# Kernel tuning notes

Measured on AMD Instinct MI355X. Metric: run time of the kernel, lower is better.

## Reference

```python
import jax, jax.numpy as jnp
import numpy as np

N = 50000        # nodes
E = 1_600_000    # edges
F_IN = 128
HID = 128
OUT = 128
NEG_SLOPE = 0.2  # PyG GATConv default


def _gat_layer(x, src, dst, W, a_src, a_dst, b, n_nodes):
    """PyG GATConv (heads=1, add_self_loops handled by caller)."""
    h = x @ W                                   # [N, d_out]
    alpha_src = h @ a_src                       # [N]
    alpha_dst = h @ a_dst                       # [N]
    e = jax.nn.leaky_relu(alpha_src[src] + alpha_dst[dst], NEG_SLOPE)  # [E']
    # segment softmax over incoming edges of each destination node
    m = jax.ops.segment_max(e, dst, num_segments=n_nodes)
    e = jnp.exp(e - m[dst])
    s = jax.ops.segment_sum(e, dst, num_segments=n_nodes)
    alpha = e / s[dst]                          # [E']
    out = jax.ops.segment_sum(alpha[:, None] * h[src], dst, num_segments=n_nodes)
    return out + b


def setup_inputs() -> dict:
    key = jax.random.key(0)
    ks = jax.random.split(key, 11)
    sW1 = 1.0 / np.sqrt(F_IN)
    sW2 = 1.0 / np.sqrt(HID)
    return {
        "x": jax.random.normal(ks[0], (N, F_IN), dtype=jnp.float32),
        "edge_index": jax.random.randint(ks[1], (2, E), 0, N, dtype=jnp.int64
                                         if jax.config.jax_enable_x64 else jnp.int32),
        "W1": jax.random.normal(ks[2], (F_IN, HID), dtype=jnp.float32) * sW1,
        "a1_src": jax.random.normal(ks[3], (HID,), dtype=jnp.float32) * sW2,
        "a1_dst": jax.random.normal(ks[4], (HID,), dtype=jnp.float32) * sW2,
        "b1": jnp.zeros((HID,), dtype=jnp.float32),
        "W2": jax.random.normal(ks[5], (HID, OUT), dtype=jnp.float32) * sW2,
        "a2_src": jax.random.normal(ks[6], (OUT,), dtype=jnp.float32) * sW2,
        "a2_dst": jax.random.normal(ks[7], (OUT,), dtype=jnp.float32) * sW2,
        "b2": jnp.zeros((OUT,), dtype=jnp.float32),
    }


def reference(x, edge_index, W1, a1_src, a1_dst, b1, W2, a2_src, a2_dst, b2):
    n = x.shape[0]
    loop = jnp.arange(n, dtype=edge_index.dtype)
    src = jnp.concatenate([edge_index[0], loop])   # add self loops (PyG default)
    dst = jnp.concatenate([edge_index[1], loop])
    h = _gat_layer(x, src, dst, W1, a1_src, a1_dst, b1, n)
    h = jax.nn.relu(h)
    # F.dropout with training=False is identity (eval-mode reference)
    out = _gat_layer(h, src, dst, W2, a2_src, a2_dst, b2, n)
    return out
```

## Files before the change

### kernel.cpp

```cpp
#include <hip/hip_runtime.h>
#include <hip/hip_bf16.h>
#include <hip/hip_fp16.h>

#define FD 128
#define CBW 64
#define NB_MAX 1024

typedef _Float16 half8 __attribute__((ext_vector_type(8)));
typedef float f32x4 __attribute__((ext_vector_type(4)));

__global__ __launch_bounds__(256) void k_chist(const int* __restrict__ dst,
                                               int* __restrict__ ccnt, int e, int nb) {
    __shared__ int lh[NB_MAX];
    for (int i = threadIdx.x; i < nb; i += 256) lh[i] = 0;
    __syncthreads();
    for (int i = blockIdx.x * 256 + threadIdx.x; i < e; i += gridDim.x * 256)
        atomicAdd(&lh[dst[i] >> 6], 1);
    __syncthreads();
    for (int i = threadIdx.x; i < nb; i += 256) {
        int c = lh[i];
        if (c) atomicAdd(&ccnt[i], c);
    }
}

__global__ void k_cscan(const int* __restrict__ ccnt, int* __restrict__ cbase,
                        int* __restrict__ ccur, int nb, int* __restrict__ rowptr, int n) {
    __shared__ int wsum[16];
    __shared__ int woff[17];
    const int t = threadIdx.x, lane = t & 63, wid = t >> 6;
    int carry = 0;
    for (int base = 0; base < nb; base += 1024) {
        int idx = base + t;
        int v = (idx < nb) ? ccnt[idx] : 0;
        int s = v;
#pragma unroll
        for (int off = 1; off < 64; off <<= 1) {
            int u = __shfl_up(s, off, 64);
            if (lane >= off) s += u;
        }
        if (lane == 63) wsum[wid] = s;
        __syncthreads();
        if (wid == 0) {
            int w2 = (lane < 16) ? wsum[lane] : 0;
#pragma unroll
            for (int off = 1; off < 16; off <<= 1) {
                int u = __shfl_up(w2, off, 64);
                if (lane >= off) w2 += u;
            }
            if (lane < 16) woff[lane + 1] = w2;
            if (lane == 0) woff[0] = 0;
        }
        __syncthreads();
        int excl = carry + woff[wid] + (s - v);
        if (idx < nb) { cbase[idx] = excl; ccur[idx] = excl; }
        carry += woff[16];
        __syncthreads();
    }
    if (t == 0) { cbase[nb] = carry; rowptr[n] = carry; }
}

__global__ __launch_bounds__(256) void k_cscatter(const int* __restrict__ src,
                                                  const int* __restrict__ dst,
                                                  int* __restrict__ ccur,
                                                  int* __restrict__ ebuf,
                                                  int e, int nb, int nblocks) {
    __shared__ int lh[NB_MAX];
    __shared__ int lb[NB_MAX];
    const int per = (e + nblocks - 1) / nblocks;
    const int lo = blockIdx.x * per;
    const int hi = min(e, lo + per);
    const int t = threadIdx.x;
    for (int i = t; i < nb; i += 256) lh[i] = 0;
    __syncthreads();
    for (int i = lo + t; i < hi; i += 256) atomicAdd(&lh[dst[i] >> 6], 1);
    __syncthreads();
    for (int i = t; i < nb; i += 256) {
        int c = lh[i];
        lb[i] = c ? atomicAdd(&ccur[i], c) : 0;
    }
    __syncthreads();
    for (int i = t; i < nb; i += 256) lh[i] = 0;
    __syncthreads();
    for (int i = lo + t; i < hi; i += 256) {
        int d = dst[i];
        int bkt = d >> 6;
        int r = atomicAdd(&lh[bkt], 1);
        ebuf[lb[bkt] + r] = (src[i] << 6) | (d & (CBW - 1));
    }
}

__global__ __launch_bounds__(256) void k_fine(const int* __restrict__ ebuf,
                                              const int* __restrict__ cbase,
                                              int* __restrict__ rowptr,
                                              int* __restrict__ colidx, int n) {
    const int b = blockIdx.x;
    const int node0 = b * CBW;
    const int nloc = min(CBW, n - node0);
    const int beg = cbase[b], end = cbase[b + 1];
    __shared__ int fh[CBW];
    __shared__ int fo[CBW];
    const int t = threadIdx.x;
    if (t < CBW) fh[t] = 0;
    __syncthreads();
    for (int e = beg + t; e < end; e += 256) atomicAdd(&fh[ebuf[e] & (CBW - 1)], 1);
    __syncthreads();
    if (t < 64) {
        int v = fh[t];
        int s = v;
#pragma unroll
        for (int off = 1; off < 64; off <<= 1) {
            int u = __shfl_up(s, off, 64);
            if (t >= off) s += u;
        }
        fo[t] = s - v;
    }
    __syncthreads();
    if (t < nloc) rowptr[node0 + t] = beg + fo[t];
    if (t < CBW) fh[t] = 0;
    __syncthreads();
    for (int e = beg + t; e < end; e += 256) {
        int v = ebuf[e];
        int d = v & (CBW - 1);
        int r = atomicAdd(&fh[d], 1);
        colidx[beg + fo[d] + r] = v >> 6;
    }
}

__global__ __launch_bounds__(1024) void k_wt(const float* __restrict__ Wa,
                                             const float* __restrict__ Wb,
                                             __half* __restrict__ Ta,
                                             __half* __restrict__ Tb) {
    __shared__ float sw[128 * 129];
    const float* W = blockIdx.x ? Wb : Wa;
    __half* T = blockIdx.x ? Tb : Ta;
    const int t = threadIdx.x;
#pragma unroll
    for (int i = 0; i < 16; i++) {
        int idx = i * 1024 + t;
        sw[(idx >> 7) * 129 + (idx & 127)] = W[idx];
    }
    __syncthreads();
#pragma unroll
    for (int i = 0; i < 8; i++) {
        int o = i * 1024 + t;
        int c = o >> 6, kp = o & 63;
        float lo = sw[(kp * 2) * 129 + c];
        float hi = sw[(kp * 2 + 1) * 129 + c];
        *(__half2*)&T[c * 128 + kp * 2] = __floats2half2_rn(lo, hi);
    }
}

__global__ __launch_bounds__(256) void k_gemm(const float* __restrict__ X,
                                              const __half* __restrict__ Wt,
                                              const float* __restrict__ a_s,
                                              const float* __restrict__ a_d,
                                              __half* __restrict__ H,
                                              float* __restrict__ as_,
                                              float* __restrict__ ad_, int n) {
    const int t = threadIdx.x;
    const int wave = t >> 6, lane = t & 63;
    const int g = lane >> 4, c16 = lane & 15;
    const int row0 = blockIdx.x * 64 + wave * 16;

    half8 A[4];
    {
        int row = row0 + c16;
        int rc = (row < n) ? row : (n - 1);
        const float* xp = &X[(size_t)rc * 128 + g * 8];
#pragma unroll
        for (int kc = 0; kc < 4; kc++) {
            float4 x0 = *(const float4*)(xp + kc * 32);
            float4 x1 = *(const float4*)(xp + kc * 32 + 4);
            half8 a;
            a[0] = (_Float16)x0.x; a[1] = (_Float16)x0.y;
            a[2] = (_Float16)x0.z; a[3] = (_Float16)x0.w;
            a[4] = (_Float16)x1.x; a[5] = (_Float16)x1.y;
            a[6] = (_Float16)x1.z; a[7] = (_Float16)x1.w;
            A[kc] = a;
        }
    }

    f32x4 acc[8];
#pragma unroll
    for (int ct = 0; ct < 8; ct++) acc[ct] = (f32x4){0.f, 0.f, 0.f, 0.f};

#pragma unroll
    for (int ct = 0; ct < 8; ct++) {
        const __half* wp = &Wt[(ct * 16 + c16) * 128 + g * 8];
#pragma unroll
        for (int kc = 0; kc < 4; kc++) {
            half8 b = *(const half8*)(wp + kc * 32);
            acc[ct] = __builtin_amdgcn_mfma_f32_16x16x32_f16(A[kc], b, acc[ct], 0, 0, 0);
        }
    }

    float asv[8], adv[8];
#pragma unroll
    for (int ct = 0; ct < 8; ct++) {
        asv[ct] = a_s[ct * 16 + c16];
        adv[ct] = a_d[ct * 16 + c16];
    }
#pragma unroll
    for (int r = 0; r < 4; r++) {
        const int row = row0 + g * 4 + r;
        float vs = 0.f, vd = 0.f;
#pragma unroll
        for (int ct = 0; ct < 8; ct++) {
            float v = acc[ct][r];
            vs += v * asv[ct];
            vd += v * adv[ct];
            if (row < n) H[(size_t)row * 128 + ct * 16 + c16] = __float2half(v);
        }
#pragma unroll
        for (int off = 8; off; off >>= 1) {
            vs += __shfl_xor(vs, off, 16);
            vd += __shfl_xor(vd, off, 16);
        }
        if (c16 == 0 && row < n) { as_[row] = vs; ad_[row] = vd; }
    }
}

__global__ __launch_bounds__(256) void k_aggr(const __half* __restrict__ H,
                                              const float* __restrict__ as_,
                                              const float* __restrict__ ad_,
                                              const int* __restrict__ rowptr,
                                              const int* __restrict__ colidx,
                                              const float* __restrict__ bias,
                                              float* __restrict__ out, int n, int do_relu) {
    const int wid = threadIdx.x >> 6;
    const int lane = threadIdx.x & 63;
    const int node = blockIdx.x * 4 + wid;
    if (node >= n) return;
    const int q = lane >> 4;
    const int l = lane & 15;
    const int f0 = l * 8;
    const float adn = ad_[node];
    float s_acc = 0.f;
    float a0 = 0.f, a1 = 0.f, a2 = 0.f, a3 = 0.f, a4 = 0.f, a5 = 0.f, a6 = 0.f, a7 = 0.f;
    const int beg = rowptr[node], end = rowptr[node + 1];
    int i = beg + q;
    int src_n = 0; float as_n = 0.f;
    if (i < end) { src_n = colidx[i]; as_n = as_[src_n]; }
    while (i < end) {
        const int src_c = src_n; const float as_c = as_n;
        const uint4 hv = *(const uint4*)&H[(size_t)src_c * 128 + f0];
        const int i2 = i + 4;
        if (i2 < end) { src_n = colidx[i2]; as_n = as_[src_n]; }
        float e = as_c + adn;
        e = (e > 0.f) ? e : 0.2f * e;
        const float w = __expf(e);
        s_acc += w;
        float2 p;
        p = __half22float2(*(const __half2*)&hv.x); a0 += w * p.x; a1 += w * p.y;
        p = __half22float2(*(const __half2*)&hv.y); a2 += w * p.x; a3 += w * p.y;
        p = __half22float2(*(const __half2*)&hv.z); a4 += w * p.x; a5 += w * p.y;
        p = __half22float2(*(const __half2*)&hv.w); a6 += w * p.x; a7 += w * p.y;
        i = i2;
    }
    if (q == 3) {
        float e = as_[node] + adn;
        e = (e > 0.f) ? e : 0.2f * e;
        const float w = __expf(e);
        s_acc += w;
        const uint4 hv = *(const uint4*)&H[(size_t)node * 128 + f0];
        float2 p;
        p = __half22float2(*(const __half2*)&hv.x); a0 += w * p.x; a1 += w * p.y;
        p = __half22float2(*(const __half2*)&hv.y); a2 += w * p.x; a3 += w * p.y;
        p = __half22float2(*(const __half2*)&hv.z); a4 += w * p.x; a5 += w * p.y;
        p = __half22float2(*(const __half2*)&hv.w); a6 += w * p.x; a7 += w * p.y;
    }
#pragma unroll
    for (int off = 16; off <= 32; off <<= 1) {
        s_acc += __shfl_xor(s_acc, off);
        a0 += __shfl_xor(a0, off); a1 += __shfl_xor(a1, off);
        a2 += __shfl_xor(a2, off); a3 += __shfl_xor(a3, off);
        a4 += __shfl_xor(a4, off); a5 += __shfl_xor(a5, off);
        a6 += __shfl_xor(a6, off); a7 += __shfl_xor(a7, off);
    }
    if (q == 0) {
        const float inv = 1.f / s_acc;
        const float4 b0 = *(const float4*)&bias[f0];
        const float4 b1 = *(const float4*)&bias[f0 + 4];
        float4 o0, o1;
        o0.x = a0 * inv + b0.x; o0.y = a1 * inv + b0.y;
        o0.z = a2 * inv + b0.z; o0.w = a3 * inv + b0.w;
        o1.x = a4 * inv + b1.x; o1.y = a5 * inv + b1.y;
        o1.z = a6 * inv + b1.z; o1.w = a7 * inv + b1.w;
        if (do_relu) {
            o0.x = fmaxf(o0.x, 0.f); o0.y = fmaxf(o0.y, 0.f);
            o0.z = fmaxf(o0.z, 0.f); o0.w = fmaxf(o0.w, 0.f);
            o1.x = fmaxf(o1.x, 0.f); o1.y = fmaxf(o1.y, 0.f);
            o1.z = fmaxf(o1.z, 0.f); o1.w = fmaxf(o1.w, 0.f);
        }
        *(float4*)&out[(size_t)node * 128 + f0] = o0;
        *(float4*)&out[(size_t)node * 128 + f0 + 4] = o1;
    }
}

extern "C" void kernel_launch(void* const* d_in, const int* in_sizes, int n_in,
                              void* d_out, int out_size, void* d_ws, size_t ws_size,
                              hipStream_t stream) {
    const float* x   = (const float*)d_in[0];
    const int*   ei  = (const int*)d_in[1];
    const float* W1  = (const float*)d_in[2];
    const float* a1s = (const float*)d_in[3];
    const float* a1d = (const float*)d_in[4];
    const float* b1  = (const float*)d_in[5];
    const float* W2  = (const float*)d_in[6];
    const float* a2s = (const float*)d_in[7];
    const float* a2d = (const float*)d_in[8];
    const float* b2  = (const float*)d_in[9];
    float* dout = (float*)d_out;

    const int n = in_sizes[0] / FD;
    const int E = in_sizes[1] / 2;
    const int* src = ei;
    const int* dst = ei + E;
    const int NB = (n + CBW - 1) / CBW;

    __half* H     = (__half*)d_ws;
    int*    ebuf  = (int*)d_ws;
    float* as_    = (float*)((char*)d_ws + (size_t)n * FD * sizeof(__half));
    float* ad_    = as_ + n;
    int*   rowptr = (int*)(ad_ + n);
    int*   ccnt   = rowptr + (n + 1);
    int*   cbase  = ccnt + NB;
    int*   ccur   = cbase + NB + 1;
    int*   colidx = ccur + NB;
    size_t wt_off = (((size_t)((char*)(colidx + E) - (char*)d_ws)) + 15) & ~(size_t)15;
    __half* Wt1h  = (__half*)((char*)d_ws + wt_off);
    __half* Wt2h  = Wt1h + 128 * 128;

    k_wt<<<2, 1024, 0, stream>>>(W1, W2, Wt1h, Wt2h);
    hipMemsetAsync(ccnt, 0, (size_t)NB * sizeof(int), stream);
    k_chist<<<256, 256, 0, stream>>>(dst, ccnt, E, NB);
    k_cscan<<<1, 1024, 0, stream>>>(ccnt, cbase, ccur, NB, rowptr, n);
    const int SCAT_BLOCKS = 256;
    k_cscatter<<<SCAT_BLOCKS, 256, 0, stream>>>(src, dst, ccur, ebuf, E, NB, SCAT_BLOCKS);
    k_fine<<<NB, 256, 0, stream>>>(ebuf, cbase, rowptr, colidx, n);

    const int gemm_grid = (n + 63) / 64;
    const int node_grid = (n + 3) / 4;

    k_gemm<<<gemm_grid, 256, 0, stream>>>(x, Wt1h, a1s, a1d, H, as_, ad_, n);
    k_aggr<<<node_grid, 256, 0, stream>>>(H, as_, ad_, rowptr, colidx, b1, dout, n, 1);

    k_gemm<<<gemm_grid, 256, 0, stream>>>(dout, Wt2h, a2s, a2d, H, as_, ad_, n);
    k_aggr<<<node_grid, 256, 0, stream>>>(H, as_, ad_, rowptr, colidx, b2, dout, n, 0);
}
```

Baseline: 254.7 us.

## Precompute normalized attention weights in separate kernel and unroll aggregation by two

Adds a k_alpha kernel that computes per-edge exp-leaky-relu scores, normalizes them per destination and stores alpha per edge plus the self-loop weight. The aggregation kernel then reads precomputed alpha instead of gathering as_[src] and computing exp inline. It also processes two edges per lane group per iteration so more H row loads are in flight. This removes the dependent as_ gather from the latency-bound aggregation loop, at the cost of an extra kernel launch and extra per-edge alpha writes and reads.

```diff
diff --git a/kernel.cpp b/kernel.cpp
--- a/kernel.cpp
+++ b/kernel.cpp
@@ -220,9 +220,47 @@
     }
 }
 
+__global__ __launch_bounds__(256) void k_alpha(const float* __restrict__ as_,
+                                               const float* __restrict__ ad_,
+                                               const int* __restrict__ rowptr,
+                                               const int* __restrict__ colidx,
+                                               float* __restrict__ alpha,
+                                               float* __restrict__ aself, int n) {
+    const int wid = threadIdx.x >> 6;
+    const int lane = threadIdx.x & 63;
+    const int node = blockIdx.x * 4 + wid;
+    if (node >= n) return;
+    const float adn = ad_[node];
+    const int beg = rowptr[node], end = rowptr[node + 1];
+    float s = 0.f;
+    for (int i = beg + lane; i < end; i += 64) {
+        float e = as_[colidx[i]] + adn;
+        e = (e > 0.f) ? e : 0.2f * e;
+        float w = __expf(e);
+        alpha[i] = w;
+        s += w;
+    }
+    float es = as_[node] + adn;
+    es = (es > 0.f) ? es : 0.2f * es;
+    const float wself = __expf(es);
+    if (lane == 0) s += wself;
+#pragma unroll
+    for (int off = 32; off; off >>= 1) s += __shfl_xor(s, off);
+    const float inv = 1.f / s;
+    for (int i = beg + lane; i < end; i += 64) alpha[i] *= inv;
+    if (lane == 0) aself[node] = wself * inv;
+}
+
+__device__ __forceinline__ void fmix8(float* acc, uint4 hv, float w) {
+    union { uint4 u; _Float16 h[8]; } c;
+    c.u = hv;
+#pragma unroll
+    for (int j = 0; j < 8; j++) acc[j] += w * (float)c.h[j];
+}
+
 __global__ __launch_bounds__(256) void k_aggr(const __half* __restrict__ H,
-                                              const float* __restrict__ as_,
-                                              const float* __restrict__ ad_,
+                                              const float* __restrict__ alpha,
+                                              const float* __restrict__ aself,
                                               const int* __restrict__ rowptr,
                                               const int* __restrict__ colidx,
                                               const float* __restrict__ bias,
@@ -234,58 +272,45 @@
     const int q = lane >> 4;
     const int l = lane & 15;
     const int f0 = l * 8;
-    const float adn = ad_[node];
-    float s_acc = 0.f;
-    float a0 = 0.f, a1 = 0.f, a2 = 0.f, a3 = 0.f, a4 = 0.f, a5 = 0.f, a6 = 0.f, a7 = 0.f;
+    float acc[8] = {0.f, 0.f, 0.f, 0.f, 0.f, 0.f, 0.f, 0.f};
     const int beg = rowptr[node], end = rowptr[node + 1];
-    int i = beg + q;
-    int src_n = 0; float as_n = 0.f;
-    if (i < end) { src_n = colidx[i]; as_n = as_[src_n]; }
-    while (i < end) {
-        const int src_c = src_n; const float as_c = as_n;
-        const uint4 hv = *(const uint4*)&H[(size_t)src_c * 128 + f0];
-        const int i2 = i + 4;
-        if (i2 < end) { src_n = colidx[i2]; as_n = as_[src_n]; }
-        float e = as_c + adn;
-        e = (e > 0.f) ? e : 0.2f * e;
-        const float w = __expf(e);
-        s_acc += w;
-        float2 p;
-        p = __half22float2(*(const __half2*)&hv.x); a0 += w * p.x; a1 += w * p.y;
-        p = __half22float2(*(const __half2*)&hv.y); a2 += w * p.x; a3 += w * p.y;
-        p = __half22float2(*(const __half2*)&hv.z); a4 += w * p.x; a5 += w * p.y;
-        p = __half22float2(*(const __half2*)&hv.w); a6 += w * p.x; a7 += w * p.y;
-        i = i2;
+
+    int i0 = beg + q, i1 = beg + q + 4;
+    int s0 = 0, s1 = 0;
+    float w0 = 0.f, w1 = 0.f;
+    if (i0 < end) { s0 = colidx[i0]; w0 = alpha[i0]; }
+    if (i1 < end) { s1 = colidx[i1]; w1 = alpha[i1]; }
+    while (i0 < end) {
+        const uint4 h0 = *(const uint4*)&H[(size_t)s0 * 128 + f0];
+        const bool has1 = (i1 < end);
+        uint4 h1;
+        if (has1) h1 = *(const uint4*)&H[(size_t)s1 * 128 + f0];
+        const float cw0 = w0, cw1 = w1;
+        const int n0 = i0 + 8, n1 = i1 + 8;
+        if (n0 < end) { s0 = colidx[n0]; w0 = alpha[n0]; }
+        if (n1 < end) { s1 = colidx[n1]; w1 = alpha[n1]; }
+        fmix8(acc, h0, cw0);
+        if (has1) fmix8(acc, h1, cw1);
+        i0 = n0; i1 = n1;
     }
     if (q == 3) {
-        float e = as_[node] + adn;
-        e = (e > 0.f) ? e : 0.2f * e;
-        const float w = __expf(e);
-        s_acc += w;
+        const float w = aself[node];
         const uint4 hv = *(const uint4*)&H[(size_t)node * 128 + f0];
-        float2 p;
-        p = __half22float2(*(const __half2*)&hv.x); a0 += w * p.x; a1 += w * p.y;
-        p = __half22float2(*(const __half2*)&hv.y); a2 += w * p.x; a3 += w * p.y;
-        p = __half22float2(*(const __half2*)&hv.z); a4 += w * p.x; a5 += w * p.y;
-        p = __half22float2(*(const __half2*)&hv.w); a6 += w * p.x; a7 += w * p.y;
+        fmix8(acc, hv, w);
     }
 #pragma unroll
     for (int off = 16; off <= 32; off <<= 1) {
-        s_acc += __shfl_xor(s_acc, off);
-        a0 += __shfl_xor(a0, off); a1 += __shfl_xor(a1, off);
-        a2 += __shfl_xor(a2, off); a3 += __shfl_xor(a3, off);
-        a4 += __shfl_xor(a4, off); a5 += __shfl_xor(a5, off);
-        a6 += __shfl_xor(a6, off); a7 += __shfl_xor(a7, off);
+#pragma unroll
+        for (int j = 0; j < 8; j++) acc[j] += __shfl_xor(acc[j], off);
     }
     if (q == 0) {
-        const float inv = 1.f / s_acc;
         const float4 b0 = *(const float4*)&bias[f0];
         const float4 b1 = *(const float4*)&bias[f0 + 4];
         float4 o0, o1;
-        o0.x = a0 * inv + b0.x; o0.y = a1 * inv + b0.y;
-        o0.z = a2 * inv + b0.z; o0.w = a3 * inv + b0.w;
-        o1.x = a4 * inv + b1.x; o1.y = a5 * inv + b1.y;
-        o1.z = a6 * inv + b1.z; o1.w = a7 * inv + b1.w;
+        o0.x = acc[0] + b0.x; o0.y = acc[1] + b0.y;
+        o0.z = acc[2] + b0.z; o0.w = acc[3] + b0.w;
+        o1.x = acc[4] + b1.x; o1.y = acc[5] + b1.y;
+        o1.z = acc[6] + b1.z; o1.w = acc[7] + b1.w;
         if (do_relu) {
             o0.x = fmaxf(o0.x, 0.f); o0.y = fmaxf(o0.y, 0.f);
             o0.z = fmaxf(o0.z, 0.f); o0.w = fmaxf(o0.w, 0.f);
@@ -322,12 +347,14 @@
     int*    ebuf  = (int*)d_ws;
     float* as_    = (float*)((char*)d_ws + (size_t)n * FD * sizeof(__half));
     float* ad_    = as_ + n;
-    int*   rowptr = (int*)(ad_ + n);
+    float* aself  = ad_ + n;
+    int*   rowptr = (int*)(aself + n);
     int*   ccnt   = rowptr + (n + 1);
     int*   cbase  = ccnt + NB;
     int*   ccur   = cbase + NB + 1;
     int*   colidx = ccur + NB;
-    size_t wt_off = (((size_t)((char*)(colidx + E) - (char*)d_ws)) + 15) & ~(size_t)15;
+    float* alpha  = (float*)(colidx + E);
+    size_t wt_off = (((size_t)((char*)(alpha + E) - (char*)d_ws)) + 15) & ~(size_t)15;
     __half* Wt1h  = (__half*)((char*)d_ws + wt_off);
     __half* Wt2h  = Wt1h + 128 * 128;
 
@@ -343,8 +370,10 @@
     const int node_grid = (n + 3) / 4;
 
     k_gemm<<<gemm_grid, 256, 0, stream>>>(x, Wt1h, a1s, a1d, H, as_, ad_, n);
-    k_aggr<<<node_grid, 256, 0, stream>>>(H, as_, ad_, rowptr, colidx, b1, dout, n, 1);
+    k_alpha<<<node_grid, 256, 0, stream>>>(as_, ad_, rowptr, colidx, alpha, aself, n);
+    k_aggr<<<node_grid, 256, 0, stream>>>(H, alpha, aself, rowptr, colidx, b1, dout, n, 1);
 
     k_gemm<<<gemm_grid, 256, 0, stream>>>(dout, Wt2h, a2s, a2d, H, as_, ad_, n);
-    k_aggr<<<node_grid, 256, 0, stream>>>(H, as_, ad_, rowptr, colidx, b2, dout, n, 0);
-}
+    k_alpha<<<node_grid, 256, 0, stream>>>(as_, ad_, rowptr, colidx, alpha, aself, n);
+    k_aggr<<<node_grid, 256, 0, stream>>>(H, alpha, aself, rowptr, colidx, b2, dout, n, 0);
+}
```

Result: slower. 266.5 us (+4.6%).

## Feed GEMMs fp16 activations and batch 16 edge gathers per aggregation iteration

Applied to the files above, without the earlier changes.

Adds a kernel that converts x to fp16 once. The first aggregation now writes its ReLU output directly as fp16 into a dedicated buffer, so both GEMMs read half-precision inputs instead of fp32. The aggregation loop now issues four independent H-row gathers per lane per iteration (16 edges per wave) and prefetches the next batch's indices and attention scores, to hide gather latency. The cost is an extra conversion pass over x, a larger workspace with a separate H buffer, higher register pressure, and fp16 rounding of the intermediate activations.

```diff
diff --git a/kernel.cpp b/kernel.cpp
--- a/kernel.cpp
+++ b/kernel.cpp
@@ -150,7 +150,21 @@
     }
 }
 
-__global__ __launch_bounds__(256) void k_gemm(const float* __restrict__ X,
+__global__ __launch_bounds__(256) void k_x16(const float* __restrict__ x,
+                                             __half* __restrict__ y, int count8) {
+    int i = blockIdx.x * 256 + threadIdx.x;
+    if (i >= count8) return;
+    float4 a = *(const float4*)&x[(size_t)i * 8];
+    float4 b = *(const float4*)&x[(size_t)i * 8 + 4];
+    union { __half2 h2[4]; uint4 u; } pk;
+    pk.h2[0] = __floats2half2_rn(a.x, a.y);
+    pk.h2[1] = __floats2half2_rn(a.z, a.w);
+    pk.h2[2] = __floats2half2_rn(b.x, b.y);
+    pk.h2[3] = __floats2half2_rn(b.z, b.w);
+    *(uint4*)&y[(size_t)i * 8] = pk.u;
+}
+
+__global__ __launch_bounds__(256) void k_gemm(const __half* __restrict__ X,
                                               const __half* __restrict__ Wt,
                                               const float* __restrict__ a_s,
                                               const float* __restrict__ a_d,
@@ -166,18 +180,9 @@
     {
         int row = row0 + c16;
         int rc = (row < n) ? row : (n - 1);
-        const float* xp = &X[(size_t)rc * 128 + g * 8];
-#pragma unroll
-        for (int kc = 0; kc < 4; kc++) {
-            float4 x0 = *(const float4*)(xp + kc * 32);
-            float4 x1 = *(const float4*)(xp + kc * 32 + 4);
-            half8 a;
-            a[0] = (_Float16)x0.x; a[1] = (_Float16)x0.y;
-            a[2] = (_Float16)x0.z; a[3] = (_Float16)x0.w;
-            a[4] = (_Float16)x1.x; a[5] = (_Float16)x1.y;
-            a[6] = (_Float16)x1.z; a[7] = (_Float16)x1.w;
-            A[kc] = a;
-        }
+        const __half* xp = &X[(size_t)rc * 128 + g * 8];
+#pragma unroll
+        for (int kc = 0; kc < 4; kc++) A[kc] = *(const half8*)(xp + kc * 32);
     }
 
     f32x4 acc[8];
@@ -218,6 +223,13 @@
         }
         if (c16 == 0 && row < n) { as_[row] = vs; ad_[row] = vd; }
     }
+}
+
+__device__ __forceinline__ void fmix8(float* acc, uint4 hv, float w) {
+    union { uint4 u; _Float16 h[8]; } c;
+    c.u = hv;
+#pragma unroll
+    for (int j = 0; j < 8; j++) acc[j] += w * (float)c.h[j];
 }
 
 __global__ __launch_bounds__(256) void k_aggr(const __half* __restrict__ H,
@@ -226,7 +238,9 @@
                                               const int* __restrict__ rowptr,
                                               const int* __restrict__ colidx,
                                               const float* __restrict__ bias,
-                                              float* __restrict__ out, int n, int do_relu) {
+                                              float* __restrict__ outf,
+                                              __half* __restrict__ outh,
+                                              int n, int mode) {
     const int wid = threadIdx.x >> 6;
     const int lane = threadIdx.x & 63;
     const int node = blockIdx.x * 4 + wid;
@@ -236,64 +250,82 @@
     const int f0 = l * 8;
     const float adn = ad_[node];
     float s_acc = 0.f;
-    float a0 = 0.f, a1 = 0.f, a2 = 0.f, a3 = 0.f, a4 = 0.f, a5 = 0.f, a6 = 0.f, a7 = 0.f;
+    float acc[8] = {0.f, 0.f, 0.f, 0.f, 0.f, 0.f, 0.f, 0.f};
     const int beg = rowptr[node], end = rowptr[node + 1];
-    int i = beg + q;
-    int src_n = 0; float as_n = 0.f;
-    if (i < end) { src_n = colidx[i]; as_n = as_[src_n]; }
-    while (i < end) {
-        const int src_c = src_n; const float as_c = as_n;
-        const uint4 hv = *(const uint4*)&H[(size_t)src_c * 128 + f0];
-        const int i2 = i + 4;
-        if (i2 < end) { src_n = colidx[i2]; as_n = as_[src_n]; }
-        float e = as_c + adn;
-        e = (e > 0.f) ? e : 0.2f * e;
-        const float w = __expf(e);
-        s_acc += w;
-        float2 p;
-        p = __half22float2(*(const __half2*)&hv.x); a0 += w * p.x; a1 += w * p.y;
-        p = __half22float2(*(const __half2*)&hv.y); a2 += w * p.x; a3 += w * p.y;
-        p = __half22float2(*(const __half2*)&hv.z); a4 += w * p.x; a5 += w * p.y;
-        p = __half22float2(*(const __half2*)&hv.w); a6 += w * p.x; a7 += w * p.y;
-        i = i2;
-    }
+
     if (q == 3) {
         float e = as_[node] + adn;
         e = (e > 0.f) ? e : 0.2f * e;
         const float w = __expf(e);
         s_acc += w;
-        const uint4 hv = *(const uint4*)&H[(size_t)node * 128 + f0];
-        float2 p;
-        p = __half22float2(*(const __half2*)&hv.x); a0 += w * p.x; a1 += w * p.y;
-        p = __half22float2(*(const __half2*)&hv.y); a2 += w * p.x; a3 += w * p.y;
-        p = __half22float2(*(const __half2*)&hv.z); a4 += w * p.x; a5 += w * p.y;
-        p = __half22float2(*(const __half2*)&hv.w); a6 += w * p.x; a7 += w * p.y;
-    }
+        fmix8(acc, *(const uint4*)&H[(size_t)node * 128 + f0], w);
+    }
+
+    int it = beg;
+    int s[4]; float a[4];
+#pragma unroll
+    for (int j = 0; j < 4; j++) {
+        int idx = it + q + 4 * j;
+        s[j] = node; a[j] = -1e30f;
+        if (idx < end) { s[j] = colidx[idx]; a[j] = as_[s[j]]; }
+    }
+    while (it < end) {
+        uint4 h[4]; float w[4];
+#pragma unroll
+        for (int j = 0; j < 4; j++) {
+            int idx = it + q + 4 * j;
+            h[j] = make_uint4(0u, 0u, 0u, 0u);
+            if (idx < end) h[j] = *(const uint4*)&H[(size_t)s[j] * 128 + f0];
+        }
+#pragma unroll
+        for (int j = 0; j < 4; j++) {
+            float e = a[j] + adn;
+            e = (e > 0.f) ? e : 0.2f * e;
+            w[j] = __expf(e);
+        }
+        const int nit = it + 16;
+        int ns[4]; float na[4];
+#pragma unroll
+        for (int j = 0; j < 4; j++) {
+            int idx = nit + q + 4 * j;
+            ns[j] = node; na[j] = -1e30f;
+            if (idx < end) { ns[j] = colidx[idx]; na[j] = as_[ns[j]]; }
+        }
+#pragma unroll
+        for (int j = 0; j < 4; j++) { s_acc += w[j]; fmix8(acc, h[j], w[j]); }
+#pragma unroll
+        for (int j = 0; j < 4; j++) { s[j] = ns[j]; a[j] = na[j]; }
+        it = nit;
+    }
+
 #pragma unroll
     for (int off = 16; off <= 32; off <<= 1) {
         s_acc += __shfl_xor(s_acc, off);
-        a0 += __shfl_xor(a0, off); a1 += __shfl_xor(a1, off);
-        a2 += __shfl_xor(a2, off); a3 += __shfl_xor(a3, off);
-        a4 += __shfl_xor(a4, off); a5 += __shfl_xor(a5, off);
-        a6 += __shfl_xor(a6, off); a7 += __shfl_xor(a7, off);
+#pragma unroll
+        for (int j = 0; j < 8; j++) acc[j] += __shfl_xor(acc[j], off);
     }
     if (q == 0) {
         const float inv = 1.f / s_acc;
+        float o[8];
         const float4 b0 = *(const float4*)&bias[f0];
         const float4 b1 = *(const float4*)&bias[f0 + 4];
-        float4 o0, o1;
-        o0.x = a0 * inv + b0.x; o0.y = a1 * inv + b0.y;
-        o0.z = a2 * inv + b0.z; o0.w = a3 * inv + b0.w;
-        o1.x = a4 * inv + b1.x; o1.y = a5 * inv + b1.y;
-        o1.z = a6 * inv + b1.z; o1.w = a7 * inv + b1.w;
-        if (do_relu) {
-            o0.x = fmaxf(o0.x, 0.f); o0.y = fmaxf(o0.y, 0.f);
-            o0.z = fmaxf(o0.z, 0.f); o0.w = fmaxf(o0.w, 0.f);
-            o1.x = fmaxf(o1.x, 0.f); o1.y = fmaxf(o1.y, 0.f);
-            o1.z = fmaxf(o1.z, 0.f); o1.w = fmaxf(o1.w, 0.f);
-        }
-        *(float4*)&out[(size_t)node * 128 + f0] = o0;
-        *(float4*)&out[(size_t)node * 128 + f0 + 4] = o1;
+        o[0] = acc[0] * inv + b0.x; o[1] = acc[1] * inv + b0.y;
+        o[2] = acc[2] * inv + b0.z; o[3] = acc[3] * inv + b0.w;
+        o[4] = acc[4] * inv + b1.x; o[5] = acc[5] * inv + b1.y;
+        o[6] = acc[6] * inv + b1.z; o[7] = acc[7] * inv + b1.w;
+        if (mode == 1) {
+#pragma unroll
+            for (int j = 0; j < 8; j++) o[j] = fmaxf(o[j], 0.f);
+            union { __half2 h2[4]; uint4 u; } pk;
+            pk.h2[0] = __floats2half2_rn(o[0], o[1]);
+            pk.h2[1] = __floats2half2_rn(o[2], o[3]);
+            pk.h2[2] = __floats2half2_rn(o[4], o[5]);
+            pk.h2[3] = __floats2half2_rn(o[6], o[7]);
+            *(uint4*)&outh[(size_t)node * 128 + f0] = pk.u;
+        } else {
+            *(float4*)&outf[(size_t)node * 128 + f0] = make_float4(o[0], o[1], o[2], o[3]);
+            *(float4*)&outf[(size_t)node * 128 + f0 + 4] = make_float4(o[4], o[5], o[6], o[7]);
+        }
     }
 }
 
@@ -318,17 +350,19 @@
     const int* dst = ei + E;
     const int NB = (n + CBW - 1) / CBW;
 
-    __half* H     = (__half*)d_ws;
-    int*    ebuf  = (int*)d_ws;
-    float* as_    = (float*)((char*)d_ws + (size_t)n * FD * sizeof(__half));
+    char* base = (char*)d_ws;
+    __half* buf0  = (__half*)base;
+    int*    ebuf  = (int*)base;
+    __half* H     = (__half*)(base + (size_t)n * FD * sizeof(__half));
+    float* as_    = (float*)((char*)H + (size_t)n * FD * sizeof(__half));
     float* ad_    = as_ + n;
     int*   rowptr = (int*)(ad_ + n);
     int*   ccnt   = rowptr + (n + 1);
     int*   cbase  = ccnt + NB;
     int*   ccur   = cbase + NB + 1;
     int*   colidx = ccur + NB;
-    size_t wt_off = (((size_t)((char*)(colidx + E) - (char*)d_ws)) + 15) & ~(size_t)15;
-    __half* Wt1h  = (__half*)((char*)d_ws + wt_off);
+    size_t wt_off = (((size_t)((char*)(colidx + E) - base)) + 15) & ~(size_t)15;
+    __half* Wt1h  = (__half*)(base + wt_off);
     __half* Wt2h  = Wt1h + 128 * 128;
 
     k_wt<<<2, 1024, 0, stream>>>(W1, W2, Wt1h, Wt2h);
@@ -339,12 +373,17 @@
     k_cscatter<<<SCAT_BLOCKS, 256, 0, stream>>>(src, dst, ccur, ebuf, E, NB, SCAT_BLOCKS);
     k_fine<<<NB, 256, 0, stream>>>(ebuf, cbase, rowptr, colidx, n);
 
+    const int count8 = n * FD / 8;
+    k_x16<<<(count8 + 255) / 256, 256, 0, stream>>>(x, buf0, count8);
+
     const int gemm_grid = (n + 63) / 64;
     const int node_grid = (n + 3) / 4;
 
-    k_gemm<<<gemm_grid, 256, 0, stream>>>(x, Wt1h, a1s, a1d, H, as_, ad_, n);
-    k_aggr<<<node_grid, 256, 0, stream>>>(H, as_, ad_, rowptr, colidx, b1, dout, n, 1);
-
-    k_gemm<<<gemm_grid, 256, 0, stream>>>(dout, Wt2h, a2s, a2d, H, as_, ad_, n);
-    k_aggr<<<node_grid, 256, 0, stream>>>(H, as_, ad_, rowptr, colidx, b2, dout, n, 0);
-}
+    k_gemm<<<gemm_grid, 256, 0, stream>>>(buf0, Wt1h, a1s, a1d, H, as_, ad_, n);
+    k_aggr<<<node_grid, 256, 0, stream>>>(H, as_, ad_, rowptr, colidx, b1,
+                                          nullptr, buf0, n, 1);
+
+    k_gemm<<<gemm_grid, 256, 0, stream>>>(buf0, Wt2h, a2s, a2d, H, as_, ad_, n);
+    k_aggr<<<node_grid, 256, 0, stream>>>(H, as_, ad_, rowptr, colidx, b2,
+                                          dout, nullptr, n, 0);
+}
```

Result: faster. 245.1 us (-3.8%).
